# Performance work log

Measured on AMD Instinct MI355X. Metric: run time of the kernel, lower is better.

Reference implementation:

```python
import jax, jax.numpy as jnp
import numpy as np

ACTION_DIM = 4
OBS_DIM = 10
A0_WEIGHT = 10.0
TARGET_WEIGHT = 3.0


def setup_inputs() -> dict:
    key = jax.random.key(0)
    k1, k2 = jax.random.split(key)
    shape = (16, 32, 2564)  # bs, horizon, action_dim + n_entities*obs_dim
    preds = jax.random.normal(k1, shape, dtype=jnp.float32)
    targ = jax.random.normal(k2, shape, dtype=jnp.float32)
    return {"preds": preds, "targ": targ}


def reference(preds, targ):
    bs, horizon, _ = preds.shape
    # ---- action loss ----
    actions = preds[:, :, :ACTION_DIM]
    action_targs = targ[:, :, :ACTION_DIM]
    action_l1 = jnp.abs(actions - action_targs).mean(axis=-1)  # [bs, horizon]
    a0_loss = action_l1[:, 1].mean()
    action_l1 = action_l1.at[:, 1].multiply(A0_WEIGHT)
    action_loss = action_l1.mean()
    # ---- chamfer over entities ----
    obs = preds[:, :, ACTION_DIM:].reshape(bs * horizon, -1, OBS_DIM)      # [B', N, 10]
    obs_targ = targ[:, :, ACTION_DIM:].reshape(bs * horizon, -1, OBS_DIM)
    feat = obs[..., 5:9]          # identity features, [B', N, 4]
    feat_t = obs_targ[..., 5:9]
    # l2_simple pairwise distances: [B', N, N]
    P = jnp.sum((feat[:, :, None, :] - feat_t[:, None, :, :]) ** 2, axis=-1)
    # direction 1: for each target point, closest pred point (min over axis 1)
    idx1 = jnp.argmin(P, axis=1)  # [B', N]
    aligned_obs = jnp.take_along_axis(obs, idx1[..., None], axis=1)  # [B', N, 10]
    particle_dist1 = jnp.abs(aligned_obs - obs_targ)
    # direction 2: for each pred point, closest target point (min over axis 2)
    idx2 = jnp.argmin(P, axis=2)  # [B', N]
    aligned_obs_targ = jnp.take_along_axis(obs_targ, idx2[..., None], axis=1)
    particle_dist2 = jnp.abs(aligned_obs_targ - obs)
    chamfer = (TARGET_WEIGHT * particle_dist1 + particle_dist2) / (TARGET_WEIGHT + 1.0)
    loss = action_loss + chamfer.mean()
    return (loss, a0_loss)
```

## Files before the change

### kernel.cpp

```cpp
#include <hip/hip_runtime.h>

#define NP 256
#define OD 10
#define ROWLEN 2564
#define NB 512

__global__ __launch_bounds__(256) void cham_main(const float* __restrict__ preds,
                                                 const float* __restrict__ targ,
                                                 float* __restrict__ ws) {
    const int b = blockIdx.x;
    const int t = threadIdx.x;
    const int base = b * ROWLEN;

    __shared__ float sA[4][NP];
    __shared__ float sB[4][NP];

    float rA[4], rB[4];
#pragma unroll
    for (int d = 0; d < 4; ++d) {
        float a  = preds[base + 4 + t * OD + 5 + d];
        float bb = targ [base + 4 + t * OD + 5 + d];
        sA[d][t] = a;
        sB[d][t] = bb;
        rA[d] = a;
        rB[d] = bb;
    }
    __syncthreads();

    float best2 = 3.4e38f, best1 = 3.4e38f;
    int idx2 = 0, idx1 = 0;
#pragma unroll 4
    for (int k = 0; k < NP; ++k) {
        float d2 = 0.f, d1 = 0.f;
#pragma unroll
        for (int d = 0; d < 4; ++d) {
            float va = rA[d] - sB[d][k];
            float vb = sA[d][k] - rB[d];
            d2 = fmaf(va, va, d2);
            d1 = fmaf(vb, vb, d1);
        }
        if (d2 < best2) { best2 = d2; idx2 = k; }
        if (d1 < best1) { best1 = d1; idx1 = k; }
    }

    const int ob = base + 4;
    float s1 = 0.f, s2 = 0.f;
#pragma unroll
    for (int d = 0; d < OD; ++d) {
        float o_t   = preds[ob + t * OD + d];
        float ot_t  = targ [ob + t * OD + d];
        float o_i1  = preds[ob + idx1 * OD + d];
        float ot_i2 = targ [ob + idx2 * OD + d];
        s1 += fabsf(o_i1 - ot_t);
        s2 += fabsf(ot_i2 - o_t);
    }
    float v = 3.0f * s1 + s2;

#pragma unroll
    for (int off = 32; off > 0; off >>= 1) v += __shfl_down(v, off, 64);

    __shared__ float wsum[4];
    if ((t & 63) == 0) wsum[t >> 6] = v;
    __syncthreads();
    if (t == 0) {
        ws[b] = wsum[0] + wsum[1] + wsum[2] + wsum[3];
        float l1 = 0.f;
#pragma unroll
        for (int d = 0; d < 4; ++d) l1 += fabsf(preds[base + d] - targ[base + d]);
        l1 *= 0.25f;
        const int h = b & 31;
        ws[NB + b] = (h == 1) ? l1 * 10.0f : l1;
    }
}

__global__ __launch_bounds__(512) void cham_final(const float* __restrict__ ws,
                                                  float* __restrict__ out) {
    const int t = threadIdx.x;
    float cham = ws[t];
    float act  = ws[NB + t];
    float a0 = ((t & 31) == 1) ? act * 0.1f : 0.f;

#pragma unroll
    for (int off = 32; off > 0; off >>= 1) {
        cham += __shfl_down(cham, off, 64);
        act  += __shfl_down(act,  off, 64);
        a0   += __shfl_down(a0,   off, 64);
    }
    __shared__ float sc[8], sa[8], s0[8];
    if ((t & 63) == 0) { int w = t >> 6; sc[w] = cham; sa[w] = act; s0[w] = a0; }
    __syncthreads();
    if (t == 0) {
        float C = 0.f, A = 0.f, Z = 0.f;
#pragma unroll
        for (int w = 0; w < 8; ++w) { C += sc[w]; A += sa[w]; Z += s0[w]; }
        const float cham_mean = C * (1.0f / (4.0f * (float)NB * (float)NP * (float)OD));
        out[0] = A * (1.0f / (float)NB) + cham_mean;
        out[1] = Z * (1.0f / 16.0f);
    }
}

extern "C" void kernel_launch(void* const* d_in, const int* in_sizes, int n_in,
                              void* d_out, int out_size, void* d_ws, size_t ws_size,
                              hipStream_t stream) {
    const float* preds = (const float*)d_in[0];
    const float* targ  = (const float*)d_in[1];
    float* ws  = (float*)d_ws;
    float* out = (float*)d_out;

    cham_main <<<NB, 256, 0, stream>>>(preds, targ, ws);
    cham_final<<<1, 512, 0, stream>>>(ws, out);
}
```

Before: 85.33 us.

## Process two batch rows per block, two points per thread with float4 LDS

Each 256-thread block now handles two batch elements, with 128 threads per element and each thread computing nearest neighbours for two points. Features are stored in shared memory as float4, so each inner-loop LDS read is a vector load reused across both points. Branchy argmin updates become selects, and the final L1 gather uses float2 loads. The grid is halved to 256 blocks, which lowers parallelism on a GPU with many CUs in exchange for more ILP per thread.

```diff
diff --git a/kernel.cpp b/kernel.cpp
--- a/kernel.cpp
+++ b/kernel.cpp
@@ -4,57 +4,79 @@
 #define OD 10
 #define ROWLEN 2564
 #define NB 512
+#define FINF 3.4e38f
 
 __global__ __launch_bounds__(256) void cham_main(const float* __restrict__ preds,
                                                  const float* __restrict__ targ,
                                                  float* __restrict__ ws) {
-    const int b = blockIdx.x;
     const int t = threadIdx.x;
+    const int s = t >> 7;
+    const int u = t & 127;
+    const int b = 2 * blockIdx.x + s;
     const int base = b * ROWLEN;
+    const int ob = base + 4;
 
-    __shared__ float sA[4][NP];
-    __shared__ float sB[4][NP];
+    __shared__ float4 sFA[2][NP];
+    __shared__ float4 sFB[2][NP];
 
-    float rA[4], rB[4];
+    float4 a[2], p[2];
 #pragma unroll
-    for (int d = 0; d < 4; ++d) {
-        float a  = preds[base + 4 + t * OD + 5 + d];
-        float bb = targ [base + 4 + t * OD + 5 + d];
-        sA[d][t] = a;
-        sB[d][t] = bb;
-        rA[d] = a;
-        rB[d] = bb;
+    for (int j = 0; j < 2; ++j) {
+        const int pp = u + 128 * j;
+        const int fo = ob + pp * OD + 5;
+        float4 av = make_float4(preds[fo], preds[fo + 1], preds[fo + 2], preds[fo + 3]);
+        float4 pv = make_float4(targ[fo], targ[fo + 1], targ[fo + 2], targ[fo + 3]);
+        a[j] = av; p[j] = pv;
+        sFA[s][pp] = av;
+        sFB[s][pp] = pv;
     }
     __syncthreads();
 
-    float best2 = 3.4e38f, best1 = 3.4e38f;
-    int idx2 = 0, idx1 = 0;
+    float bd2[2] = {FINF, FINF}, bd1[2] = {FINF, FINF};
+    int   id2[2] = {0, 0},       id1[2] = {0, 0};
+
 #pragma unroll 4
     for (int k = 0; k < NP; ++k) {
-        float d2 = 0.f, d1 = 0.f;
+        const float4 fb = sFB[s][k];
+        const float4 fa = sFA[s][k];
 #pragma unroll
-        for (int d = 0; d < 4; ++d) {
-            float va = rA[d] - sB[d][k];
-            float vb = sA[d][k] - rB[d];
-            d2 = fmaf(va, va, d2);
-            d1 = fmaf(vb, vb, d1);
+        for (int j = 0; j < 2; ++j) {
+            float dx0 = a[j].x - fb.x, dx1 = a[j].y - fb.y,
+                  dx2 = a[j].z - fb.z, dx3 = a[j].w - fb.w;
+            float d2 = fmaf(dx0, dx0, fmaf(dx1, dx1, fmaf(dx2, dx2, dx3 * dx3)));
+            bool c2 = d2 < bd2[j];
+            bd2[j] = c2 ? d2 : bd2[j];
+            id2[j] = c2 ? k : id2[j];
+
+            float ex0 = fa.x - p[j].x, ex1 = fa.y - p[j].y,
+                  ex2 = fa.z - p[j].z, ex3 = fa.w - p[j].w;
+            float d1 = fmaf(ex0, ex0, fmaf(ex1, ex1, fmaf(ex2, ex2, ex3 * ex3)));
+            bool c1 = d1 < bd1[j];
+            bd1[j] = c1 ? d1 : bd1[j];
+            id1[j] = c1 ? k : id1[j];
         }
-        if (d2 < best2) { best2 = d2; idx2 = k; }
-        if (d1 < best1) { best1 = d1; idx1 = k; }
     }
 
-    const int ob = base + 4;
-    float s1 = 0.f, s2 = 0.f;
+    const float2* pr2 = (const float2*)(preds + ob);
+    const float2* tg2 = (const float2*)(targ + ob);
+    float v = 0.f;
 #pragma unroll
-    for (int d = 0; d < OD; ++d) {
-        float o_t   = preds[ob + t * OD + d];
-        float ot_t  = targ [ob + t * OD + d];
-        float o_i1  = preds[ob + idx1 * OD + d];
-        float ot_i2 = targ [ob + idx2 * OD + d];
-        s1 += fabsf(o_i1 - ot_t);
-        s2 += fabsf(ot_i2 - o_t);
+    for (int j = 0; j < 2; ++j) {
+        const int rc = u + 128 * j;
+        const float2* po = pr2 + rc * 5;
+        const float2* to = tg2 + rc * 5;
+        const float2* pg = pr2 + id1[j] * 5;
+        const float2* tg = tg2 + id2[j] * 5;
+        float s1 = 0.f, s2 = 0.f;
+#pragma unroll
+        for (int d = 0; d < 5; ++d) {
+            float2 x1 = pg[d], y1 = to[d];
+            s1 += fabsf(x1.x - y1.x) + fabsf(x1.y - y1.y);
+            float2 x2 = tg[d], y2 = po[d];
+            s2 += fabsf(x2.x - y2.x) + fabsf(x2.y - y2.y);
+        }
+        v += 3.0f * s1 + s2;
     }
-    float v = 3.0f * s1 + s2;
 
 #pragma unroll
     for (int off = 32; off > 0; off >>= 1) v += __shfl_down(v, off, 64);
@@ -62,8 +84,9 @@
     __shared__ float wsum[4];
     if ((t & 63) == 0) wsum[t >> 6] = v;
     __syncthreads();
-    if (t == 0) {
-        ws[b] = wsum[0] + wsum[1] + wsum[2] + wsum[3];
+    if ((t & 127) == 0) {
+        const int w = t >> 6;
+        ws[b] = wsum[w] + wsum[w + 1];
         float l1 = 0.f;
 #pragma unroll
         for (int d = 0; d < 4; ++d) l1 += fabsf(preds[base + d] - targ[base + d]);
@@ -107,6 +130,6 @@
     float* ws  = (float*)d_ws;
     float* out = (float*)d_out;
 
-    cham_main <<<NB, 256, 0, stream>>>(preds, targ, ws);
+    cham_main <<<256, 256, 0, stream>>>(preds, targ, ws);
     cham_final<<<1, 512, 0, stream>>>(ws, out);
 }
```

After: 90.47 us. 1.06x slower.
